# Kernel optimization log

Measured on AMD Instinct MI355X. Metric: run time of the kernel, lower is better.

Reference implementation:

```python
import jax, jax.numpy as jnp
import numpy as np

BLANK = 0
T, N, C, S = 1024, 64, 128, 128


def setup_inputs() -> dict:
    key = jax.random.key(0)
    k1, k2, k3, k4 = jax.random.split(key, 4)
    logits = jax.random.normal(k1, (T, N, C), dtype=jnp.float32)
    log_probs = jax.nn.log_softmax(logits, axis=-1)
    targets = jax.random.randint(k2, (N, S), 1, C).astype(jnp.int64)  # non-blank labels
    input_lengths = jax.random.randint(k3, (N,), T // 2, T + 1).astype(jnp.int32)
    target_lengths = jax.random.randint(k4, (N,), S // 2, S + 1).astype(jnp.int32)
    return {"log_probs": log_probs, "targets": targets,
            "input_lengths": input_lengths, "target_lengths": target_lengths}


def _ctc_loss(log_probs, targets, input_lengths, target_lengths):
    Tt, Nn, Cc = log_probs.shape
    Ss = targets.shape[1]
    Sx = 2 * Ss + 1  # extended target length (blanks interleaved)
    neg_inf = jnp.asarray(-jnp.inf, log_probs.dtype)

    ext = jnp.full((Nn, Sx), BLANK, dtype=jnp.int32).at[:, 1::2].set(targets.astype(jnp.int32))
    # emission log-prob of each extended state at each time: [T, N, Sx]
    emit = jnp.take_along_axis(log_probs, jnp.broadcast_to(ext[None], (Tt, Nn, Sx)), axis=2)
    # skip transition allowed when label[s] != label[s-2] (and s >= 2)
    skip = jnp.concatenate([jnp.zeros((Nn, 2), bool), ext[:, 2:] != ext[:, :-2]], axis=1)

    # faithful to the torch code: alphas initialized to ZEROS, then states 0,1 set
    alpha0 = jnp.zeros((Nn, Sx), log_probs.dtype)
    alpha0 = alpha0.at[:, 0].set(emit[0, :, 0]).at[:, 1].set(emit[0, :, 1])

    pad1 = jnp.full((Nn, 1), neg_inf, log_probs.dtype)
    pad2 = jnp.full((Nn, 2), neg_inf, log_probs.dtype)

    def step(alpha, emit_t):
        a_m1 = jnp.concatenate([pad1, alpha[:, :-1]], axis=1)
        a_m2 = jnp.where(skip, jnp.concatenate([pad2, alpha[:, :-2]], axis=1), neg_inf)
        new = jax.nn.logsumexp(jnp.stack([alpha, a_m1, a_m2]), axis=0) + emit_t
        return new, new

    _, rest = jax.lax.scan(step, alpha0, emit[1:])
    alphas = jnp.concatenate([alpha0[None], rest], axis=0)  # [T, N, Sx]

    n_idx = jnp.arange(Nn)
    v = alphas[input_lengths - 1, n_idx, 2 * target_lengths - 1]  # [N]
    # original: loss = -logsumexp over batch, then .mean() of a scalar (identity)
    return -jax.nn.logsumexp(v)


def reference(log_probs, targets, input_lengths, target_lengths):
    return _ctc_loss(log_probs, targets, input_lengths, target_lengths)
```

## Files before the change

### kernel.cpp

```cpp
#include <hip/hip_runtime.h>
#include <math.h>

#define TT 1024
#define NN 64
#define CC 128
#define SS 128
#define CH 32
#define NCHUNK 32

#define DPP_QP_XOR1   0xB1
#define DPP_QP_XOR2   0x4E
#define DPP_WAVE_SHR1 0x138
#define DPP_ROW_MIRR  0x140
#define DPP_HALF_MIRR 0x141
#define DPP_BCAST15   0x142
#define DPP_BCAST31   0x143

template <int CTRL>
__device__ __forceinline__ float dpp_max_stage(float v) {
    int p = __builtin_amdgcn_update_dpp(__float_as_int(v), __float_as_int(v),
                                        CTRL, 0xF, 0xF, false);
    return fmaxf(v, __int_as_float(p));
}

__device__ __forceinline__ float dpp_shr1(float v) {
    int p = __builtin_amdgcn_update_dpp(0, __float_as_int(v),
                                        DPP_WAVE_SHR1, 0xF, 0xF, true);
    return __int_as_float(p);
}

__global__ __launch_bounds__(192) void ctc_scan(
    const float* __restrict__ lp,
    const int*   __restrict__ targets,
    const int*   __restrict__ ilen,
    const int*   __restrict__ tlen,
    float*       __restrict__ v_out)
{
    const int n    = blockIdx.x;
    const int tid  = threadIdx.x;
    const int wv   = tid >> 6;
    const int lane = tid & 63;

    __shared__ float s_pa[2][CH][64];
    __shared__ float s_pc[2][CH][64];
    __shared__ float s_pb[2][CH];

    const int tgA = targets[n * SS + 2 * lane];
    const int tgB = targets[n * SS + 2 * lane + 1];
    const float* lpn = lp + (size_t)n * CC;

    if (wv != 0) {
        const int w = wv - 1;
        float va[16], vc[16];
#pragma unroll
        for (int i = 0; i < 16; ++i) {
            const int j = 2 * i + w;
            const float* row = lpn + (size_t)(1 + j) * (NN * CC);
            va[i] = row[tgA]; vc[i] = row[tgB];
        }
        float pbv = 0.f;
        if (w == 0 && lane < CH) pbv = lpn[(size_t)(1 + lane) * (NN * CC)];
#pragma unroll
        for (int i = 0; i < 16; ++i) {
            const int j = 2 * i + w;
            s_pa[0][j][lane] = __expf(va[i]);
            s_pc[0][j][lane] = __expf(vc[i]);
        }
        if (w == 0 && lane < CH) s_pb[0][lane] = __expf(pbv);
    }

    const int tgBm = (lane > 0) ? targets[n * SS + 2 * lane - 1] : -1;
    const float k1f = (lane > 0 && tgA != tgBm) ? 1.f : 0.f;
    const float k3f = (tgB != tgA) ? 1.f : 0.f;
    const int il    = ilen[n];
    const int vs    = 2 * tlen[n] - 1;
    const int vlane = vs >> 2;

    float a0 = 1.f, a1 = 1.f, a2 = 1.f, a3 = 1.f, ls = 0.f;
    if (wv == 0) {
        a0 = (lane == 0) ? __expf(lpn[0])   : 1.f;
        a1 = (lane == 0) ? __expf(lpn[tgA]) : 1.f;
    }
    float a3p = (lane == 0) ? 0.f : 1.f;
    float mr = 1.f, inv = 1.f;

    __syncthreads();

    for (int cc = 0; cc < NCHUNK; ++cc) {
        const int b = cc & 1;
        if (wv == 0) {
            const int t0 = 1 + cc * CH;
            float qa[4], qc[4], qb[4];
#pragma unroll
            for (int k = 0; k < 4; ++k) {
                qa[k] = s_pa[b][k][lane];
                qc[k] = s_pc[b][k][lane];
                qb[k] = s_pb[b][k];
            }
#pragma unroll
            for (int j = 0; j < CH; ++j) {
                const int sl = j & 3;
                const float cpa = qa[sl], cpc = qc[sl], cpb = qb[sl];
                if (j + 4 < CH) {
                    qa[sl] = s_pa[b][j + 4][lane];
                    qc[sl] = s_pc[b][j + 4][lane];
                    qb[sl] = s_pb[b][j + 4];
                }

                float nb3 = fmaf(k3f, a1, a3 + a2) * cpc;
                float a3pn = dpp_shr1(nb3);
                float nb0 = (a0 + a3p) * cpb;
                float nb1 = fmaf(k1f, a3p, a0 + a1) * cpa;
                float nb2 = (a2 + a1) * cpb;

                const int jj = j & 7;
                if      (jj == 0) mr = fmaxf(fmaxf(nb0, nb1), fmaxf(nb2, nb3));
                else if (jj == 1) mr = dpp_max_stage<DPP_QP_XOR1>(mr);
                else if (jj == 2) mr = dpp_max_stage<DPP_QP_XOR2>(mr);
                else if (jj == 3) mr = dpp_max_stage<DPP_HALF_MIRR>(mr);
                else if (jj == 4) mr = dpp_max_stage<DPP_ROW_MIRR>(mr);
                else if (jj == 5) mr = dpp_max_stage<DPP_BCAST15>(mr);
                else if (jj == 6) mr = dpp_max_stage<DPP_BCAST31>(mr);
                else {
                    const float mru = __int_as_float(
                        __builtin_amdgcn_readlane(__float_as_int(mr), 63));
                    inv = 1.0f / mru;
                    ls += __logf(mru);
                    nb0 *= inv; nb1 *= inv; nb2 *= inv; nb3 *= inv;
                }

                const int t = t0 + j;
                if (t == il - 1) {
                    if (lane == vlane) v_out[n] = __logf((vs & 2) ? nb3 : nb1) + ls;
                }

                a0 = nb0; a1 = nb1; a2 = nb2; a3 = nb3;
                if (jj == 7) a3pn *= inv;
                a3p = a3pn;
            }
        } else if (cc + 1 < NCHUNK) {
            const int w  = wv - 1;
            const int b2 = (cc + 1) & 1;
            const int t0 = 1 + (cc + 1) * CH;
            float va[16], vc[16];
#pragma unroll
            for (int i = 0; i < 16; ++i) {
                const int j = 2 * i + w;
                int t = t0 + j; if (t > TT - 1) t = TT - 1;
                const float* row = lpn + (size_t)t * (NN * CC);
                va[i] = row[tgA]; vc[i] = row[tgB];
            }
            float pbv = 0.f;
            if (w == 0 && lane < CH) {
                int t = t0 + lane; if (t > TT - 1) t = TT - 1;
                pbv = lpn[(size_t)t * (NN * CC)];
            }
#pragma unroll
            for (int i = 0; i < 16; ++i) {
                const int j = 2 * i + w;
                s_pa[b2][j][lane] = __expf(va[i]);
                s_pc[b2][j][lane] = __expf(vc[i]);
            }
            if (w == 0 && lane < CH) s_pb[b2][lane] = __expf(pbv);
        }
        __syncthreads();
    }
}

__global__ void ctc_reduce(const float* __restrict__ v, float* __restrict__ out)
{
    const int lane = threadIdx.x;
    float x = v[lane];
    float m = x;
#pragma unroll
    for (int off = 32; off > 0; off >>= 1) m = fmaxf(m, __shfl_xor(m, off));
    float e = __expf(x - m);
#pragma unroll
    for (int off = 32; off > 0; off >>= 1) e += __shfl_xor(e, off);
    if (lane == 0) out[0] = -(m + __logf(e));
}

extern "C" void kernel_launch(void* const* d_in, const int* in_sizes, int n_in,
                              void* d_out, int out_size, void* d_ws, size_t ws_size,
                              hipStream_t stream) {
    const float* lp      = (const float*)d_in[0];
    const int*   targets = (const int*)d_in[1];
    const int*   ilen    = (const int*)d_in[2];
    const int*   tlen    = (const int*)d_in[3];

    float* v   = (float*)d_ws;
    float* out = (float*)d_out;

    ctc_scan<<<NN, 192, 0, stream>>>(lp, targets, ilen, tlen, v);
    ctc_reduce<<<1, 64, 0, stream>>>(v, out);
}
```

Measured before the change: 85.12 us.

## Pack emission probs into float4 LDS and use four producer waves

Emission values for two timesteps (label A and label B) are now interleaved into float4 shared-memory entries, and blank probabilities into float4 groups. The scan wave then reads them with wide LDS loads instead of three scalar loads per step. The producer side grows from two to four waves (320 threads), so each wave issues fewer gathers per chunk and the prefetch of the next chunk should finish sooner behind the sequential recurrence. The costs are more threads per block and more register selects to unpack the float4 components.

```diff
diff --git a/kernel.cpp b/kernel.cpp
--- a/kernel.cpp
+++ b/kernel.cpp
@@ -29,7 +29,7 @@
     return __int_as_float(p);
 }
 
-__global__ __launch_bounds__(192) void ctc_scan(
+__global__ __launch_bounds__(320) void ctc_scan(
     const float* __restrict__ lp,
     const int*   __restrict__ targets,
     const int*   __restrict__ ilen,
@@ -41,9 +41,8 @@
     const int wv   = tid >> 6;
     const int lane = tid & 63;
 
-    __shared__ float s_pa[2][CH][64];
-    __shared__ float s_pc[2][CH][64];
-    __shared__ float s_pb[2][CH];
+    __shared__ float4 s_e[2][CH / 2][64];
+    __shared__ float4 s_pb4[2][CH / 4];
 
     const int tgA = targets[n * SS + 2 * lane];
     const int tgB = targets[n * SS + 2 * lane + 1];
@@ -51,22 +50,24 @@
 
     if (wv != 0) {
         const int w = wv - 1;
-        float va[16], vc[16];
-#pragma unroll
-        for (int i = 0; i < 16; ++i) {
-            const int j = 2 * i + w;
-            const float* row = lpn + (size_t)(1 + j) * (NN * CC);
-            va[i] = row[tgA]; vc[i] = row[tgB];
+        float va[8], vc[8];
+#pragma unroll
+        for (int i = 0; i < 4; ++i) {
+            const int k = w + 4 * i;
+            const float* rowa = lpn + (size_t)(1 + 2 * k) * (NN * CC);
+            const float* rowb = lpn + (size_t)(2 + 2 * k) * (NN * CC);
+            va[2*i]   = rowa[tgA]; vc[2*i]   = rowa[tgB];
+            va[2*i+1] = rowb[tgA]; vc[2*i+1] = rowb[tgB];
         }
         float pbv = 0.f;
-        if (w == 0 && lane < CH) pbv = lpn[(size_t)(1 + lane) * (NN * CC)];
-#pragma unroll
-        for (int i = 0; i < 16; ++i) {
-            const int j = 2 * i + w;
-            s_pa[0][j][lane] = __expf(va[i]);
-            s_pc[0][j][lane] = __expf(vc[i]);
+        if (lane < 8) pbv = lpn[(size_t)(1 + w * 8 + lane) * (NN * CC)];
+#pragma unroll
+        for (int i = 0; i < 4; ++i) {
+            const int k = w + 4 * i;
+            s_e[0][k][lane] = make_float4(__expf(va[2*i]),   __expf(vc[2*i]),
+                                          __expf(va[2*i+1]), __expf(vc[2*i+1]));
         }
-        if (w == 0 && lane < CH) s_pb[0][lane] = __expf(pbv);
+        if (lane < 8) ((float*)s_pb4[0])[w * 8 + lane] = __expf(pbv);
     }
 
     const int tgBm = (lane > 0) ? targets[n * SS + 2 * lane - 1] : -1;
@@ -90,78 +91,83 @@
         const int b = cc & 1;
         if (wv == 0) {
             const int t0 = 1 + cc * CH;
-            float qa[4], qc[4], qb[4];
-#pragma unroll
-            for (int k = 0; k < 4; ++k) {
-                qa[k] = s_pa[b][k][lane];
-                qc[k] = s_pc[b][k][lane];
-                qb[k] = s_pb[b][k];
-            }
-#pragma unroll
-            for (int j = 0; j < CH; ++j) {
-                const int sl = j & 3;
-                const float cpa = qa[sl], cpc = qc[sl], cpb = qb[sl];
-                if (j + 4 < CH) {
-                    qa[sl] = s_pa[b][j + 4][lane];
-                    qc[sl] = s_pc[b][j + 4][lane];
-                    qb[sl] = s_pb[b][j + 4];
+            float4 eA0 = s_e[b][0][lane], eB0 = s_e[b][1][lane], pq0 = s_pb4[b][0];
+            float4 eA1 = s_e[b][2][lane], eB1 = s_e[b][3][lane], pq1 = s_pb4[b][1];
+#pragma unroll
+            for (int m = 0; m < 8; ++m) {
+                float4 ea, eb, pq;
+                if (m & 1) { ea = eA1; eb = eB1; pq = pq1; }
+                else       { ea = eA0; eb = eB0; pq = pq0; }
+                if (m + 2 < 8) {
+                    if (m & 1) { eA1 = s_e[b][2*(m+2)][lane]; eB1 = s_e[b][2*(m+2)+1][lane]; pq1 = s_pb4[b][m+2]; }
+                    else       { eA0 = s_e[b][2*(m+2)][lane]; eB0 = s_e[b][2*(m+2)+1][lane]; pq0 = s_pb4[b][m+2]; }
                 }
-
-                float nb3 = fmaf(k3f, a1, a3 + a2) * cpc;
-                float a3pn = dpp_shr1(nb3);
-                float nb0 = (a0 + a3p) * cpb;
-                float nb1 = fmaf(k1f, a3p, a0 + a1) * cpa;
-                float nb2 = (a2 + a1) * cpb;
-
-                const int jj = j & 7;
-                if      (jj == 0) mr = fmaxf(fmaxf(nb0, nb1), fmaxf(nb2, nb3));
-                else if (jj == 1) mr = dpp_max_stage<DPP_QP_XOR1>(mr);
-                else if (jj == 2) mr = dpp_max_stage<DPP_QP_XOR2>(mr);
-                else if (jj == 3) mr = dpp_max_stage<DPP_HALF_MIRR>(mr);
-                else if (jj == 4) mr = dpp_max_stage<DPP_ROW_MIRR>(mr);
-                else if (jj == 5) mr = dpp_max_stage<DPP_BCAST15>(mr);
-                else if (jj == 6) mr = dpp_max_stage<DPP_BCAST31>(mr);
-                else {
-                    const float mru = __int_as_float(
-                        __builtin_amdgcn_readlane(__float_as_int(mr), 63));
-                    inv = 1.0f / mru;
-                    ls += __logf(mru);
-                    nb0 *= inv; nb1 *= inv; nb2 *= inv; nb3 *= inv;
+#pragma unroll
+                for (int c = 0; c < 4; ++c) {
+                    const int j   = 4 * m + c;
+                    const float cpa = (c==0)?ea.x:(c==1)?ea.z:(c==2)?eb.x:eb.z;
+                    const float cpc = (c==0)?ea.y:(c==1)?ea.w:(c==2)?eb.y:eb.w;
+                    const float cpb = (c==0)?pq.x:(c==1)?pq.y:(c==2)?pq.z:pq.w;
+
+                    float nb3 = fmaf(k3f, a1, a3 + a2) * cpc;
+                    float a3pn = dpp_shr1(nb3);
+                    float nb0 = (a0 + a3p) * cpb;
+                    float nb1 = fmaf(k1f, a3p, a0 + a1) * cpa;
+                    float nb2 = (a2 + a1) * cpb;
+
+                    const int jj = j & 7;
+                    if      (jj == 0) mr = fmaxf(fmaxf(nb0, nb1), fmaxf(nb2, nb3));
+                    else if (jj == 1) mr = dpp_max_stage<DPP_QP_XOR1>(mr);
+                    else if (jj == 2) mr = dpp_max_stage<DPP_QP_XOR2>(mr);
+                    else if (jj == 3) mr = dpp_max_stage<DPP_HALF_MIRR>(mr);
+                    else if (jj == 4) mr = dpp_max_stage<DPP_ROW_MIRR>(mr);
+                    else if (jj == 5) mr = dpp_max_stage<DPP_BCAST15>(mr);
+                    else if (jj == 6) mr = dpp_max_stage<DPP_BCAST31>(mr);
+                    else {
+                        const float mru = __int_as_float(
+                            __builtin_amdgcn_readlane(__float_as_int(mr), 63));
+                        inv = 1.0f / mru;
+                        ls += __logf(mru);
+                        nb0 *= inv; nb1 *= inv; nb2 *= inv; nb3 *= inv;
+                    }
+
+                    const int t = t0 + j;
+                    if (t == il - 1) {
+                        if (lane == vlane) v_out[n] = __logf((vs & 2) ? nb3 : nb1) + ls;
+                    }
+
+                    a0 = nb0; a1 = nb1; a2 = nb2; a3 = nb3;
+                    if (jj == 7) a3pn *= inv;
+                    a3p = a3pn;
                 }
-
-                const int t = t0 + j;
-                if (t == il - 1) {
-                    if (lane == vlane) v_out[n] = __logf((vs & 2) ? nb3 : nb1) + ls;
-                }
-
-                a0 = nb0; a1 = nb1; a2 = nb2; a3 = nb3;
-                if (jj == 7) a3pn *= inv;
-                a3p = a3pn;
             }
         } else if (cc + 1 < NCHUNK) {
             const int w  = wv - 1;
             const int b2 = (cc + 1) & 1;
             const int t0 = 1 + (cc + 1) * CH;
-            float va[16], vc[16];
-#pragma unroll
-            for (int i = 0; i < 16; ++i) {
-                const int j = 2 * i + w;
-                int t = t0 + j; if (t > TT - 1) t = TT - 1;
-                const float* row = lpn + (size_t)t * (NN * CC);
-                va[i] = row[tgA]; vc[i] = row[tgB];
+            float va[8], vc[8];
+#pragma unroll
+            for (int i = 0; i < 4; ++i) {
+                const int k = w + 4 * i;
+                int ta = t0 + 2 * k;     if (ta > TT - 1) ta = TT - 1;
+                int tb = t0 + 2 * k + 1; if (tb > TT - 1) tb = TT - 1;
+                const float* rowa = lpn + (size_t)ta * (NN * CC);
+                const float* rowb = lpn + (size_t)tb * (NN * CC);
+                va[2*i]   = rowa[tgA]; vc[2*i]   = rowa[tgB];
+                va[2*i+1] = rowb[tgA]; vc[2*i+1] = rowb[tgB];
             }
             float pbv = 0.f;
-            if (w == 0 && lane < CH) {
-                int t = t0 + lane; if (t > TT - 1) t = TT - 1;
-                pbv = lpn[(size_t)t * (NN * CC)];
-            }
-#pragma unroll
-            for (int i = 0; i < 16; ++i) {
-                const int j = 2 * i + w;
-                s_pa[b2][j][lane] = __expf(va[i]);
-                s_pc[b2][j][lane] = __expf(vc[i]);
-            }
-            if (w == 0 && lane < CH) s_pb[b2][lane] = __expf(pbv);
+            if (lane < 8) {
+                int tp = t0 + w * 8 + lane; if (tp > TT - 1) tp = TT - 1;
+                pbv = lpn[(size_t)tp * (NN * CC)];
+            }
+#pragma unroll
+            for (int i = 0; i < 4; ++i) {
+                const int k = w + 4 * i;
+                s_e[b2][k][lane] = make_float4(__expf(va[2*i]),   __expf(vc[2*i]),
+                                               __expf(va[2*i+1]), __expf(vc[2*i+1]));
+            }
+            if (lane < 8) ((float*)s_pb4[b2])[w * 8 + lane] = __expf(pbv);
         }
         __syncthreads();
     }
@@ -191,6 +197,6 @@
     float* v   = (float*)d_ws;
     float* out = (float*)d_out;
 
-    ctc_scan<<<NN, 192, 0, stream>>>(lp, targets, ilen, tlen, v);
+    ctc_scan<<<NN, 320, 0, stream>>>(lp, targets, ilen, tlen, v);
     ctc_reduce<<<1, 64, 0, stream>>>(v, out);
 }
```

Result: faster. 71.71 us (-15.8%).
